# Kernel tuning notes

Measured on AMD Instinct MI355X. Metric: run time of the kernel, lower is better.

## Reference

```python
import jax, jax.numpy as jnp
import numpy as np

B, C_IN, H, W = 4, 256, 200, 176
A = 6            # anchors per location (3 sizes x 2 rotations)
NUM_CLS = 4      # 3 classes + background
K = 100
N_ANCH = A * H * W


def setup_inputs() -> dict:
    key = jax.random.key(0)
    k1, k2, k3, k4, k5, k6 = jax.random.split(key, 6)
    x = jax.random.normal(k1, (B, C_IN, H, W), dtype=jnp.float32)
    scale = 1.0 / np.sqrt(C_IN)
    cls_w = jax.random.normal(k2, (NUM_CLS * A, C_IN), dtype=jnp.float32) * scale
    cls_b = jnp.zeros((NUM_CLS * A,), dtype=jnp.float32)
    reg_w = jax.random.normal(k3, (7 * A, C_IN), dtype=jnp.float32) * scale * 0.1
    reg_b = jnp.zeros((7 * A,), dtype=jnp.float32)
    # anchors: [N,7] = (x, y, z, dx, dy, dz, ry) with strictly positive sizes
    xyz = jax.random.uniform(k4, (N_ANCH, 3), minval=-35.0, maxval=35.0)
    sizes = jax.random.uniform(k5, (N_ANCH, 3), minval=1.0, maxval=4.0)
    rot = jax.random.uniform(k6, (N_ANCH, 1), minval=-np.pi, maxval=np.pi)
    anchors = jnp.concatenate([xyz, sizes, rot], axis=-1).astype(jnp.float32)
    return {"x": x, "cls_w": cls_w, "cls_b": cls_b,
            "reg_w": reg_w, "reg_b": reg_b, "anchors": anchors}


def _decode(deltas, anchors):
    # SECOND-style residual box decoder.  deltas, anchors: [B, N, 7]
    xa, ya, za, dxa, dya, dza, ra = jnp.split(anchors, 7, axis=-1)
    xt, yt, zt, dxt, dyt, dzt, rt = jnp.split(deltas, 7, axis=-1)
    diag = jnp.sqrt(dxa * dxa + dya * dya)
    xg = xt * diag + xa
    yg = yt * diag + ya
    zg = zt * dza + za
    dxg = jnp.exp(dxt) * dxa
    dyg = jnp.exp(dyt) * dya
    dzg = jnp.exp(dzt) * dza
    rg = rt + ra
    return jnp.concatenate([xg, yg, zg, dxg, dyg, dzg, rg], axis=-1)


def reference(x, cls_w, cls_b, reg_w, reg_b, anchors):
    # 1x1 conv heads: [B,C_in,H,W] -> [B,C_out,H,W]
    cls_pred = jnp.einsum('bchw,oc->bohw', x, cls_w) + cls_b[None, :, None, None]
    reg_pred = jnp.einsum('bchw,oc->bohw', x, reg_w) + reg_b[None, :, None, None]
    # permute(0,2,3,1).reshape(B, num_anchors, -1)
    cls_pred = jnp.transpose(cls_pred, (0, 2, 3, 1)).reshape(B, N_ANCH, NUM_CLS)
    reg_pred = jnp.transpose(reg_pred, (0, 2, 3, 1)).reshape(B, N_ANCH, 7)
    batch_anchors = jnp.broadcast_to(anchors[None], (B, N_ANCH, 7))
    pred_bboxes = _decode(reg_pred, batch_anchors)
    pred_scores = jax.nn.softmax(cls_pred, axis=-1)
    # per-frame top-k over max foreground score (classes 1:)
    max_scores = jnp.max(pred_scores[..., 1:], axis=-1)      # [B, N]
    _, topk_inds = jax.lax.top_k(max_scores, K)              # [B, K]
    topk_bboxes = jnp.take_along_axis(pred_bboxes, topk_inds[..., None], axis=1)
    topk_scores = jnp.take_along_axis(pred_scores, topk_inds[..., None], axis=1)
    return (topk_scores, topk_bboxes)
```

## Files before the change

kernel.cpp:

```cpp
#include <hip/hip_runtime.h>

#define BB 4
#define CIN 256
#define HW 35200
#define AA 6
#define NANCH (AA * HW)
#define TOPK 100
#define NBIN 4096
#define BINBASE 28416
#define CAP 4096
#define SMAX 4096
#define TILES 138
#define ZEROWORDS (BB * NBIN + 16)

__device__ __forceinline__ unsigned sbin(unsigned bits) {
  int v = (int)(bits >> 15) - BINBASE;
  v = v < 0 ? 0 : v;
  v = v > (NBIN - 1) ? (NBIN - 1) : v;
  return (unsigned)v;
}

__device__ __forceinline__ float sc4(float4 l) {
  float m = fmaxf(fmaxf(l.x, l.y), fmaxf(l.z, l.w));
  float e0 = expf(l.x - m), e1 = expf(l.y - m);
  float e2 = expf(l.z - m), e3 = expf(l.w - m);
  return fmaxf(fmaxf(e1, e2), e3) / (e0 + e1 + e2 + e3);
}

#define FMA4(A, W, S)                                      \
  A.x = fmaf(S, W.x, A.x); A.y = fmaf(S, W.y, A.y);        \
  A.z = fmaf(S, W.z, A.z); A.w = fmaf(S, W.w, A.w);

__global__ __launch_bounds__(256) void k0_init(
    const float* __restrict__ cls_w, float* __restrict__ wt,
    unsigned int* __restrict__ zr) {
  int t = blockIdx.x * 256 + threadIdx.x;
  int stride = gridDim.x * 256;
  for (int i = t; i < ZEROWORDS; i += stride) zr[i] = 0u;
  for (int i = t; i < 24 * CIN; i += stride)
    wt[(i % CIN) * 24 + (i / CIN)] = cls_w[i];
}

__global__ __launch_bounds__(256, 4) void k1_scores(
    const float* __restrict__ x, const float* __restrict__ wt,
    const float* __restrict__ cls_b, unsigned int* __restrict__ hist,
    float* __restrict__ maxsc) {
  int bid = blockIdx.x;
  int b = bid / TILES, tile = bid % TILES;
  int tid = threadIdx.x;

  __shared__ unsigned lh[NBIN];
  for (int i = tid; i < NBIN; i += 256) lh[i] = 0;
  __syncthreads();

  int hwg = tile * 256 + tid;
  bool act = hwg < HW;
  int hwc = act ? hwg : (HW - 1);
  const float* xb = x + (size_t)b * CIN * HW + hwc;

  float4 a0 = make_float4(cls_b[0], cls_b[1], cls_b[2], cls_b[3]);
  float4 a1 = make_float4(cls_b[4], cls_b[5], cls_b[6], cls_b[7]);
  float4 a2 = make_float4(cls_b[8], cls_b[9], cls_b[10], cls_b[11]);
  float4 a3 = make_float4(cls_b[12], cls_b[13], cls_b[14], cls_b[15]);
  float4 a4 = make_float4(cls_b[16], cls_b[17], cls_b[18], cls_b[19]);
  float4 a5 = make_float4(cls_b[20], cls_b[21], cls_b[22], cls_b[23]);

#pragma unroll 1
  for (int cc = 0; cc < CIN; cc += 16) {
    float xv[16];
#pragma unroll
    for (int u = 0; u < 16; ++u)
      xv[u] = xb[(size_t)(cc + u) * HW];
#pragma unroll
    for (int u = 0; u < 16; ++u) {
      const float4* wr = (const float4*)(wt + (cc + u) * 24);
      float4 w0 = wr[0], w1 = wr[1], w2 = wr[2];
      float4 w3 = wr[3], w4 = wr[4], w5 = wr[5];
      float s = xv[u];
      FMA4(a0, w0, s) FMA4(a1, w1, s) FMA4(a2, w2, s)
      FMA4(a3, w3, s) FMA4(a4, w4, s) FMA4(a5, w5, s)
    }
  }

  if (act) {
    float s0 = sc4(a0), s1 = sc4(a1), s2 = sc4(a2);
    float s3 = sc4(a3), s4 = sc4(a4), s5 = sc4(a5);
    float* mp = maxsc + (size_t)b * NANCH + (size_t)hwg * 6u;
    mp[0] = s0; mp[1] = s1; mp[2] = s2; mp[3] = s3; mp[4] = s4; mp[5] = s5;
    atomicAdd(&lh[sbin(__float_as_uint(s0))], 1u);
    atomicAdd(&lh[sbin(__float_as_uint(s1))], 1u);
    atomicAdd(&lh[sbin(__float_as_uint(s2))], 1u);
    atomicAdd(&lh[sbin(__float_as_uint(s3))], 1u);
    atomicAdd(&lh[sbin(__float_as_uint(s4))], 1u);
    atomicAdd(&lh[sbin(__float_as_uint(s5))], 1u);
  }
  __syncthreads();
  unsigned* gh = hist + (size_t)b * NBIN;
  for (int i = tid; i < NBIN; i += 256) {
    unsigned c = lh[i];
    if (c) atomicAdd(&gh[i], c);
  }
}

__global__ __launch_bounds__(256) void k2_thresh(
    const unsigned int* __restrict__ hist, unsigned int* __restrict__ thresh) {
  int b = blockIdx.x, tid = threadIdx.x;
  const unsigned* h = hist + (size_t)b * NBIN;
  unsigned r[16];
  unsigned s = 0;
#pragma unroll
  for (int i = 0; i < 16; ++i) { r[i] = h[tid * 16 + i]; s += r[i]; }
  __shared__ unsigned seg[256];
  seg[tid] = s;
  __syncthreads();
  for (int d = 1; d < 256; d <<= 1) {
    unsigned add = (tid + d < 256) ? seg[tid + d] : 0u;
    __syncthreads();
    seg[tid] += add;
    __syncthreads();
  }
  unsigned above = (tid < 255) ? seg[tid + 1] : 0u;
  if (above < TOPK && above + s >= TOPK) {
    unsigned c = above, T = 0;
    for (int i = 15; i >= 0; --i) {
      c += r[i];
      if (c >= TOPK) { T = tid * 16u + (unsigned)i; break; }
    }
    thresh[b] = T;
  }
}

__global__ __launch_bounds__(256) void k3_compact(
    const float* __restrict__ maxsc, const unsigned int* __restrict__ thresh,
    unsigned int* __restrict__ cand_count, unsigned long long* __restrict__ cand) {
  unsigned p = blockIdx.x * 256u + threadIdx.x;
  unsigned b = p / NANCH, n = p % NANCH;
  unsigned bits = __float_as_uint(maxsc[p]);
  bool pred = sbin(bits) >= thresh[b];
  unsigned long long mask = __ballot(pred);
  if (mask) {
    int lane = threadIdx.x & 63;
    int leader = (int)__ffsll(mask) - 1;
    unsigned base = 0;
    if (lane == leader)
      base = atomicAdd(&cand_count[b], (unsigned)__popcll(mask));
    base = __shfl(base, leader, 64);
    if (pred) {
      unsigned pos = base + (unsigned)__popcll(mask & ((1ull << lane) - 1ull));
      if (pos < CAP)
        cand[(size_t)b * CAP + pos] =
            ((unsigned long long)bits << 32) | (unsigned)(~n);
    }
  }
}

__global__ __launch_bounds__(256) void k4_sort(
    const unsigned long long* __restrict__ cand,
    const unsigned int* __restrict__ cand_count, unsigned int* __restrict__ topk) {
  int b = blockIdx.x, tid = threadIdx.x;
  __shared__ unsigned long long sh[SMAX];
  unsigned cnt = cand_count[b];
  if (cnt > CAP) cnt = CAP;
  unsigned S = 128;
  while (S < cnt) S <<= 1;
  for (unsigned t = tid; t < S; t += 256)
    sh[t] = (t < cnt) ? cand[(size_t)b * CAP + t] : 0ULL;
  __syncthreads();
  for (unsigned kk = 2; kk <= S; kk <<= 1) {
    for (unsigned jj = kk >> 1; jj > 0; jj >>= 1) {
      for (unsigned t = tid; t < S; t += 256) {
        unsigned ixj = t ^ jj;
        if (ixj > t) {
          unsigned long long a = sh[t], c = sh[ixj];
          bool sw = ((t & kk) == 0) ? (a < c) : (a > c);
          if (sw) { sh[t] = c; sh[ixj] = a; }
        }
      }
      __syncthreads();
    }
  }
  if (tid < TOPK)
    topk[b * TOPK + tid] = ~(unsigned)(sh[tid] & 0xFFFFFFFFULL);
}

__global__ __launch_bounds__(256) void k5_out(
    const float* __restrict__ x, const float* __restrict__ cls_w,
    const float* __restrict__ cls_b, const float* __restrict__ reg_w,
    const float* __restrict__ reg_b, const float* __restrict__ anchors,
    const unsigned int* __restrict__ topk, float* __restrict__ out) {
  int bk = blockIdx.x;
  int b = bk / TOPK, k = bk % TOPK;
  unsigned n = topk[b * TOPK + k];
  int a = (int)(n % AA);
  unsigned hw = n / AA;
  int tid = threadIdx.x;

  float xv = x[(size_t)b * CIN * HW + (size_t)tid * HW + hw];
  float part[11];
#pragma unroll
  for (int j = 0; j < 4; ++j) part[j] = xv * cls_w[(a * 4 + j) * CIN + tid];
#pragma unroll
  for (int j = 0; j < 7; ++j) part[4 + j] = xv * reg_w[(a * 7 + j) * CIN + tid];

#pragma unroll
  for (int j = 0; j < 11; ++j) {
    float v = part[j];
    for (int off = 32; off > 0; off >>= 1) v += __shfl_down(v, off, 64);
    part[j] = v;
  }
  __shared__ float red[4][11];
  int wave = tid >> 6, lane = tid & 63;
  if (lane == 0) {
#pragma unroll
    for (int j = 0; j < 11; ++j) red[wave][j] = part[j];
  }
  __syncthreads();
  if (tid == 0) {
    float tot[11];
#pragma unroll
    for (int j = 0; j < 11; ++j)
      tot[j] = red[0][j] + red[1][j] + red[2][j] + red[3][j];
    float l0 = tot[0] + cls_b[a * 4 + 0];
    float l1 = tot[1] + cls_b[a * 4 + 1];
    float l2 = tot[2] + cls_b[a * 4 + 2];
    float l3 = tot[3] + cls_b[a * 4 + 3];
    float m = fmaxf(fmaxf(l0, l1), fmaxf(l2, l3));
    float e0 = expf(l0 - m), e1 = expf(l1 - m);
    float e2 = expf(l2 - m), e3 = expf(l3 - m);
    float inv = 1.0f / (e0 + e1 + e2 + e3);
    float* os = out + ((size_t)b * TOPK + k) * 4;
    os[0] = e0 * inv; os[1] = e1 * inv; os[2] = e2 * inv; os[3] = e3 * inv;
    const float* an = anchors + (size_t)n * 7;
    float xa = an[0], ya = an[1], za = an[2];
    float dxa = an[3], dya = an[4], dza = an[5], ra = an[6];
    float xt = tot[4] + reg_b[a * 7 + 0];
    float yt = tot[5] + reg_b[a * 7 + 1];
    float zt = tot[6] + reg_b[a * 7 + 2];
    float dxt = tot[7] + reg_b[a * 7 + 3];
    float dyt = tot[8] + reg_b[a * 7 + 4];
    float dzt = tot[9] + reg_b[a * 7 + 5];
    float rt = tot[10] + reg_b[a * 7 + 6];
    float diag = sqrtf(dxa * dxa + dya * dya);
    float* ob = out + (size_t)BB * TOPK * 4 + ((size_t)b * TOPK + k) * 7;
    ob[0] = xt * diag + xa;
    ob[1] = yt * diag + ya;
    ob[2] = zt * dza + za;
    ob[3] = expf(dxt) * dxa;
    ob[4] = expf(dyt) * dya;
    ob[5] = expf(dzt) * dza;
    ob[6] = rt + ra;
  }
}

extern "C" void kernel_launch(void* const* d_in, const int* in_sizes, int n_in,
                              void* d_out, int out_size, void* d_ws, size_t ws_size,
                              hipStream_t stream) {
  const float* x       = (const float*)d_in[0];
  const float* cls_w   = (const float*)d_in[1];
  const float* cls_b   = (const float*)d_in[2];
  const float* reg_w   = (const float*)d_in[3];
  const float* reg_b   = (const float*)d_in[4];
  const float* anchors = (const float*)d_in[5];
  float* out = (float*)d_out;

  char* ws = (char*)d_ws;
  unsigned int* hist       = (unsigned int*)(ws);
  unsigned int* cand_count = (unsigned int*)(ws + 65536);
  unsigned int* thresh     = (unsigned int*)(ws + 65600);
  unsigned int* topk       = (unsigned int*)(ws + 65664);
  float* wt                = (float*)(ws + 67712);
  unsigned long long* cand = (unsigned long long*)(ws + 92288);
  float* maxsc             = (float*)(ws + 223360);

  k0_init<<<80, 256, 0, stream>>>(cls_w, wt, hist);
  k1_scores<<<BB * TILES, 256, 0, stream>>>(x, wt, cls_b, hist, maxsc);
  k2_thresh<<<BB, 256, 0, stream>>>(hist, thresh);
  k3_compact<<<(BB * NANCH) / 256, 256, 0, stream>>>(maxsc, thresh, cand_count, cand);
  k4_sort<<<BB, 256, 0, stream>>>(cand, cand_count, topk);
  k5_out<<<BB * TOPK, 256, 0, stream>>>(x, cls_w, cls_b, reg_w, reg_b, anchors,
                                        topk, out);
}
```

Measured before the change: 254.7 us.

## Split channel reduction across four waves per block with LDS reduction

The score kernel now gives each block 64 spatial positions and splits the 256 input channels across four wavefronts, 64 channels each. Partial sums go through shared memory and are reduced per anchor before softmax, the score write and the histogram update. This quadruples the block count to raise parallelism and memory-level concurrency on the bandwidth-bound 1x1 conv. In exchange it adds LDS traffic, an extra barrier and lower occupancy from the launch-bounds change. HW = 550*64 exactly, so the bounds guard is dropped.

```diff
diff --git a/kernel.cpp b/kernel.cpp
--- a/kernel.cpp
+++ b/kernel.cpp
@@ -10,7 +10,7 @@
 #define BINBASE 28416
 #define CAP 4096
 #define SMAX 4096
-#define TILES 138
+#define TILES 550
 #define ZEROWORDS (BB * NBIN + 16)
 
 __device__ __forceinline__ unsigned sbin(unsigned bits) {
@@ -41,7 +41,7 @@
     wt[(i % CIN) * 24 + (i / CIN)] = cls_w[i];
 }
 
-__global__ __launch_bounds__(256, 4) void k1_scores(
+__global__ __launch_bounds__(256, 3) void k1_scores(
     const float* __restrict__ x, const float* __restrict__ wt,
     const float* __restrict__ cls_b, unsigned int* __restrict__ hist,
     float* __restrict__ maxsc) {
@@ -50,49 +50,56 @@
   int tid = threadIdx.x;
 
   __shared__ unsigned lh[NBIN];
+  __shared__ float sred[4][64][24];
   for (int i = tid; i < NBIN; i += 256) lh[i] = 0;
-  __syncthreads();
-
-  int hwg = tile * 256 + tid;
-  bool act = hwg < HW;
-  int hwc = act ? hwg : (HW - 1);
-  const float* xb = x + (size_t)b * CIN * HW + hwc;
-
-  float4 a0 = make_float4(cls_b[0], cls_b[1], cls_b[2], cls_b[3]);
-  float4 a1 = make_float4(cls_b[4], cls_b[5], cls_b[6], cls_b[7]);
-  float4 a2 = make_float4(cls_b[8], cls_b[9], cls_b[10], cls_b[11]);
-  float4 a3 = make_float4(cls_b[12], cls_b[13], cls_b[14], cls_b[15]);
-  float4 a4 = make_float4(cls_b[16], cls_b[17], cls_b[18], cls_b[19]);
-  float4 a5 = make_float4(cls_b[20], cls_b[21], cls_b[22], cls_b[23]);
+
+  int l = tid & 63;
+  int s = __builtin_amdgcn_readfirstlane(tid >> 6);
+  int hw = tile * 64 + l;
+  const float* xb = x + (size_t)b * CIN * HW + hw;
+  int c0 = s * 64;
+
+  float4 a0 = make_float4(0.f, 0.f, 0.f, 0.f), a1 = a0, a2 = a0;
+  float4 a3 = a0, a4 = a0, a5 = a0;
 
 #pragma unroll 1
-  for (int cc = 0; cc < CIN; cc += 16) {
-    float xv[16];
-#pragma unroll
-    for (int u = 0; u < 16; ++u)
-      xv[u] = xb[(size_t)(cc + u) * HW];
-#pragma unroll
-    for (int u = 0; u < 16; ++u) {
-      const float4* wr = (const float4*)(wt + (cc + u) * 24);
+  for (int cc = 0; cc < 64; cc += 8) {
+    float xv[8];
+#pragma unroll
+    for (int u = 0; u < 8; ++u)
+      xv[u] = xb[(size_t)(c0 + cc + u) * HW];
+#pragma unroll
+    for (int u = 0; u < 8; ++u) {
+      const float4* wr = (const float4*)(wt + (c0 + cc + u) * 24);
       float4 w0 = wr[0], w1 = wr[1], w2 = wr[2];
       float4 w3 = wr[3], w4 = wr[4], w5 = wr[5];
-      float s = xv[u];
-      FMA4(a0, w0, s) FMA4(a1, w1, s) FMA4(a2, w2, s)
-      FMA4(a3, w3, s) FMA4(a4, w4, s) FMA4(a5, w5, s)
-    }
-  }
-
-  if (act) {
-    float s0 = sc4(a0), s1 = sc4(a1), s2 = sc4(a2);
-    float s3 = sc4(a3), s4 = sc4(a4), s5 = sc4(a5);
-    float* mp = maxsc + (size_t)b * NANCH + (size_t)hwg * 6u;
-    mp[0] = s0; mp[1] = s1; mp[2] = s2; mp[3] = s3; mp[4] = s4; mp[5] = s5;
-    atomicAdd(&lh[sbin(__float_as_uint(s0))], 1u);
-    atomicAdd(&lh[sbin(__float_as_uint(s1))], 1u);
-    atomicAdd(&lh[sbin(__float_as_uint(s2))], 1u);
-    atomicAdd(&lh[sbin(__float_as_uint(s3))], 1u);
-    atomicAdd(&lh[sbin(__float_as_uint(s4))], 1u);
-    atomicAdd(&lh[sbin(__float_as_uint(s5))], 1u);
+      float v = xv[u];
+      FMA4(a0, w0, v) FMA4(a1, w1, v) FMA4(a2, w2, v)
+      FMA4(a3, w3, v) FMA4(a4, w4, v) FMA4(a5, w5, v)
+    }
+  }
+
+  float4* sp = (float4*)&sred[s][l][0];
+  sp[0] = a0; sp[1] = a1; sp[2] = a2; sp[3] = a3; sp[4] = a4; sp[5] = a5;
+  __syncthreads();
+
+  const float4* bias4 = (const float4*)cls_b;
+  for (int task = tid; task < 384; task += 256) {
+    int a = task % 6, h = task / 6;
+    float4 v0 = ((const float4*)&sred[0][h][0])[a];
+    float4 v1 = ((const float4*)&sred[1][h][0])[a];
+    float4 v2 = ((const float4*)&sred[2][h][0])[a];
+    float4 v3 = ((const float4*)&sred[3][h][0])[a];
+    float4 vb = bias4[a];
+    float4 v;
+    v.x = v0.x + v1.x + v2.x + v3.x + vb.x;
+    v.y = v0.y + v1.y + v2.y + v3.y + vb.y;
+    v.z = v0.z + v1.z + v2.z + v3.z + vb.z;
+    v.w = v0.w + v1.w + v2.w + v3.w + vb.w;
+    float sc = sc4(v);
+    unsigned n = (unsigned)(tile * 64 + h) * 6u + (unsigned)a;
+    maxsc[(size_t)b * NANCH + n] = sc;
+    atomicAdd(&lh[sbin(__float_as_uint(sc))], 1u);
   }
   __syncthreads();
   unsigned* gh = hist + (size_t)b * NBIN;
```

After: 268.6 us. 1.05x slower.
